# Optimization experiments

Measured on AMD Instinct MI355X. Metric: run time of the kernel, lower is better.

The kernel has to match this reference:

```python
import jax, jax.numpy as jnp
import numpy as np

C = 256          # conv_channels
C1 = C // 2      # 128
C2 = C // 4      # 64
G = 1            # relation_glimpse


def setup_inputs() -> dict:
    key = jax.random.key(0)
    ks = jax.random.split(key, 20)
    bs, Nr, in_dim, q_dim = 4, 256, 2052, 1024
    d_in = in_dim + 4  # pos (first 4 coords) re-appended
    s = 0.02
    inp = {
        "Q": jax.random.normal(ks[0], (bs, q_dim), jnp.float32),
        "X": jax.random.normal(ks[1], (bs, Nr, in_dim), jnp.float32),
        "Wv": jax.random.normal(ks[2], (d_in, C), jnp.float32) * s,
        "bv": jnp.zeros((C,), jnp.float32),
        "Wq": jax.random.normal(ks[3], (q_dim, C), jnp.float32) * s,
        "bq": jnp.zeros((C,), jnp.float32),
        # branch 0 (r_conv01/02/03): 1x1 convs == per-position dense
        "W01": jax.random.normal(ks[4], (C, C1), jnp.float32) * s,
        "b01": jnp.zeros((C1,), jnp.float32),
        "W02": jax.random.normal(ks[5], (C1, C2), jnp.float32) * s,
        "b02": jnp.zeros((C2,), jnp.float32),
        "W03": jax.random.normal(ks[6], (C2, G), jnp.float32) * s,
        "b03": jnp.zeros((G,), jnp.float32),
        # branch 1 (r_conv1/2/3): dilation on 1x1 kernels is a no-op
        "W1": jax.random.normal(ks[7], (C, C1), jnp.float32) * s,
        "b1": jnp.zeros((C1,), jnp.float32),
        "W2": jax.random.normal(ks[8], (C1, C2), jnp.float32) * s,
        "b2": jnp.zeros((C2,), jnp.float32),
        "W3": jax.random.normal(ks[9], (C2, G), jnp.float32) * s,
        "b3": jnp.zeros((G,), jnp.float32),
    }
    return inp


def _mlp3(P, Wa, ba, Wb, bb, Wc, bc):
    # P: [bs, Nr, Nr, C]; three 1x1-conv layers, ReLU after each (incl. last).
    h = jax.nn.relu(jnp.einsum("bijc,ck->bijk", P, Wa) + ba)
    h = jax.nn.relu(jnp.einsum("bijc,ck->bijk", h, Wb) + bb)
    h = jax.nn.relu(jnp.einsum("bijc,ck->bijk", h, Wc) + bc)
    return h[..., 0]  # [bs, Nr, Nr] (relation_glimpse == 1)


def _attn_map(h):
    # symmetrize, then softmax over all Nr*Nr positions
    s = h + jnp.swapaxes(h, 1, 2)
    bs, Nr, _ = s.shape
    return jax.nn.softmax(s.reshape(bs, Nr * Nr), axis=-1).reshape(bs, Nr, Nr)


def reference(Q, X, Wv, bv, Wq, bq, W01, b01, W02, b02, W03, b03,
              W1, b1, W2, b2, W3, b3):
    X_ = X
    # append pos (first 4 coords) -> [bs, Nr, in_dim+4]
    Xcat = jnp.concatenate([X, X[:, :, :4]], axis=2)
    Xp = jnp.einsum("bnd,dc->bnc", Xcat, Wv) + bv
    Qp = Q @ Wq + bq
    Xp = Xp + Qp[:, None, :]                       # [bs, Nr, C]
    P = Xp[:, None, :, :] * Xp[:, :, None, :]      # [bs, Nr, Nr, C] pairwise product
    m0 = _attn_map(_mlp3(P, W01, b01, W02, b02, W03, b03))
    m1 = _attn_map(_mlp3(P, W1, b1, W2, b2, W3, b3))
    # weighted aggregation with original features; /(2*glimpse), then sum over Nr
    rel = jnp.einsum("bij,bjd->bid", m0 + m1, X_) / (2.0 * G)
    return rel.sum(axis=1)  # [bs, in_dim]
```

## Files before the change

kernel.cpp:

```cpp
#include <hip/hip_runtime.h>
#include <hip/hip_bf16.h>

typedef __attribute__((ext_vector_type(8)))  short short8;
typedef __attribute__((ext_vector_type(4)))  float f32x4;
typedef __attribute__((ext_vector_type(16))) float f32x16;

#define NR 256
#define CC 256

__device__ __forceinline__ unsigned short f2bf(float x) {
    union { float f; unsigned int u; } v; v.f = x;
    unsigned int r = v.u + 0x7FFFu + ((v.u >> 16) & 1u);
    return (unsigned short)(r >> 16);
}

__device__ __forceinline__ unsigned int pk2bf(float a, float b) {
    __hip_bfloat162 h = __float22bfloat162_rn(make_float2(a, b));
    union { __hip_bfloat162 h; unsigned int u; } cv; cv.h = h;
    return cv.u;
}

__global__ __launch_bounds__(256) void qp_kernel(
    const float* __restrict__ Q, const float* __restrict__ Wq,
    float* __restrict__ Qpp)
{
    const int ksl = blockIdx.x, b = blockIdx.y;
    const int n = threadIdx.x;
    __shared__ float qs[256];
    qs[n] = Q[b * 1024 + ksl * 256 + n];
    __syncthreads();
    float acc = 0.f;
    #pragma unroll 4
    for (int d = 0; d < 256; ++d) acc += qs[d] * Wq[(size_t)(ksl * 256 + d) * 256 + n];
    Qpp[(ksl * 4 + b) * 256 + n] = acc;
}

__global__ __launch_bounds__(256) void wvp_pack_kernel(
    const float* __restrict__ Wv, unsigned short* __restrict__ wvp)
{
    __shared__ float tile[32][260];
    const int ks = blockIdx.x;
    const int tid = threadIdx.x;
    for (int idx = tid; idx < 32 * 256; idx += 256) {
        int cr = idx >> 8, n = idx & 255;
        int c = ks * 32 + cr;
        tile[cr][n] = (c < 2056) ? Wv[(size_t)c * 256 + n] : 0.f;
    }
    __syncthreads();
    #pragma unroll
    for (int q = 0; q < 4; ++q) {
        int t2 = tid * 4 + q;
        int nt = t2 >> 6, l = t2 & 63;
        int gg = l >> 4, jj = l & 15;
        short8 s;
        #pragma unroll
        for (int e = 0; e < 8; ++e)
            s[e] = (short)f2bf(tile[gg * 8 + e][nt * 16 + jj]);
        *(short8*)&wvp[((size_t)(ks * 16 + nt) * 64 + l) * 8] = s;
    }
}

__global__ __launch_bounds__(256) void pack_kernel(
    const float* __restrict__ W01, const float* __restrict__ W1,
    const float* __restrict__ W02, const float* __restrict__ W2,
    unsigned short* __restrict__ wpa, unsigned short* __restrict__ wpb)
{
    int t = blockIdx.x * 256 + threadIdx.x;
    if (t < 65536) {
        int e = t & 7, l = (t >> 3) & 63, ks = (t >> 9) & 15, nt = (t >> 13) & 3, br = (t >> 15) & 1;
        int cc = ks * 16 + (l >> 5) * 8 + e;
        int n = nt * 32 + (l & 31);
        const float* W = br ? W1 : W01;
        wpa[t] = f2bf(W[cc * 128 + n]);
    } else {
        int t2 = t - 65536;
        int e = t2 & 7, l = (t2 >> 3) & 63, ks = (t2 >> 9) & 7, nt = (t2 >> 12) & 1, br = (t2 >> 13) & 1;
        int cc = ks * 16 + (l >> 5) * 8 + e;
        int n = nt * 32 + (l & 31);
        const float* W = br ? W2 : W02;
        wpb[t2] = f2bf(W[cc * 64 + n]);
    }
}

__global__ __launch_bounds__(512) void xp_kernel(
    const float* __restrict__ X, const unsigned short* __restrict__ wvp,
    const float* __restrict__ bv, const float* __restrict__ bq,
    const float* __restrict__ Qpp, float* __restrict__ Xp)
{
    __shared__ f32x4 red[8][4][65];
    const int tid = threadIdx.x;
    const int w = tid >> 6;
    const int lane = tid & 63;
    const int g = lane >> 4, j16 = lane & 15;
    const int mt = blockIdx.x;
    const int bn = blockIdx.y;
    const int b  = blockIdx.z;

    const int i0 = mt * 16;
    const int n0 = bn * 64;
    const float* xrow = X + ((size_t)(b * NR) + (i0 + j16)) * 2052;

    f32x4 acc[4] = {};

    for (int ks = w; ks < 64; ks += 8) {
        const int c0 = ks * 32 + g * 8;
        float4 xa = *(const float4*)(xrow + c0);
        float4 xb = *(const float4*)(xrow + c0 + 4);
        union { short8 s; unsigned int u[4]; } af;
        af.u[0] = pk2bf(xa.x, xa.y);
        af.u[1] = pk2bf(xa.z, xa.w);
        af.u[2] = pk2bf(xb.x, xb.y);
        af.u[3] = pk2bf(xb.z, xb.w);
        #pragma unroll
        for (int nt = 0; nt < 4; ++nt) {
            short8 bf = ((const short8*)wvp)[(size_t)(ks * 16 + bn * 4 + nt) * 64 + lane];
            acc[nt] = __builtin_amdgcn_mfma_f32_16x16x32_bf16(af.s, bf, acc[nt], 0, 0, 0);
        }
    }
    if (w == 0) {
        float xv[8];
        #pragma unroll
        for (int e = 0; e < 8; ++e) {
            int q = g * 8 + e;
            int csrc = (q < 4) ? (2048 + q) : (q - 4);
            xv[e] = xrow[csrc];
        }
        union { short8 s; unsigned int u[4]; } af;
        af.u[0] = pk2bf(xv[0], xv[1]);
        af.u[1] = pk2bf(xv[2], xv[3]);
        af.u[2] = pk2bf(xv[4], xv[5]);
        af.u[3] = pk2bf(xv[6], xv[7]);
        #pragma unroll
        for (int nt = 0; nt < 4; ++nt) {
            short8 bf = ((const short8*)wvp)[(size_t)(64 * 16 + bn * 4 + nt) * 64 + lane];
            acc[nt] = __builtin_amdgcn_mfma_f32_16x16x32_bf16(af.s, bf, acc[nt], 0, 0, 0);
        }
    }
    #pragma unroll
    for (int nt = 0; nt < 4; ++nt) red[w][nt][lane] = acc[nt];
    __syncthreads();

    {
        int nt = tid >> 7;
        int l  = tid & 63;
        int half = (tid >> 6) & 1;
        float r0 = 0.f, r1 = 0.f;
        #pragma unroll
        for (int ww = 0; ww < 8; ++ww) {
            f32x4 v = red[ww][nt][l];
            r0 += v[half * 2 + 0];
            r1 += v[half * 2 + 1];
        }
        int gg = l >> 4, jj = l & 15;
        int n = n0 + nt * 16 + jj;
        float base = bv[n] + bq[n] + Qpp[b * 256 + n] + Qpp[(4 + b) * 256 + n]
                   + Qpp[(8 + b) * 256 + n] + Qpp[(12 + b) * 256 + n];
        int row0 = i0 + gg * 4 + half * 2;
        Xp[((b * NR) + row0) * CC + n]       = r0 + base;
        Xp[((b * NR) + row0 + 1) * CC + n]   = r1 + base;
    }
}

__global__ __launch_bounds__(256, 2) void pairs_kernel(
    const float* __restrict__ Xp,
    const unsigned short* __restrict__ wpa,
    const unsigned short* __restrict__ wpb,
    const float* __restrict__ b01, const float* __restrict__ b02,
    const float* __restrict__ b03,
    const float* __restrict__ b1,  const float* __restrict__ b2,
    const float* __restrict__ b3,
    const float* __restrict__ W03, const float* __restrict__ W3,
    float* __restrict__ colpart, float* __restrict__ rowpart)
{
    __shared__ __align__(16) unsigned short lds_wa[32768];
    __shared__ __align__(16) float lds_si[1024];
    __shared__ __align__(16) float lds_bias1[128];
    __shared__ __align__(16) float lds_bias2[64];
    __shared__ __align__(16) float lds_w3[64];
    __shared__ float lds_c[4][33];

    const int tid = threadIdx.x;
    const int wave = tid >> 6;
    const int lane = tid & 63;
    const int hi = lane >> 5;
    const int j32 = lane & 31;

    int bx = blockIdx.x;
    int b = bx / 288;
    int u = bx - b * 288;
    int k = 0, off = 0;
    while (u >= off + 8 * (8 - k)) { off += 8 * (8 - k); ++k; }
    int rel = u - off, wdt = 8 - k;
    int it = k * 8 + rel / wdt;
    int jt = k + rel % wdt;

    const int i0 = it * 4;
    const int i = i0 + wave;
    const int j0 = jt * 32;
    const int br4base = b;

    {
        int ww = tid >> 6, c4 = (tid & 63) * 4;
        *(float4*)&lds_si[ww * 256 + c4] =
            *(const float4*)&Xp[((b * NR) + (i0 + ww)) * CC + c4];
    }
    __syncthreads();

    const float* xr = Xp + ((size_t)(b * NR) + (j0 + j32)) * CC;
    const float* si = lds_si + wave * 256;
    short8 bfr[16];
    #pragma unroll
    for (int ks = 0; ks < 16; ++ks) {
        const int c0 = ks * 16 + hi * 8;
        float4 xa = *(const float4*)(xr + c0);
        float4 xb = *(const float4*)(xr + c0 + 4);
        float4 sa = *(const float4*)(si + c0);
        float4 sb = *(const float4*)(si + c0 + 4);
        union { short8 s; unsigned int u[4]; } f;
        f.u[0] = pk2bf(xa.x * sa.x, xa.y * sa.y);
        f.u[1] = pk2bf(xa.z * sa.z, xa.w * sa.w);
        f.u[2] = pk2bf(xb.x * sb.x, xb.y * sb.y);
        f.u[3] = pk2bf(xb.z * sb.z, xb.w * sb.w);
        bfr[ks] = f.s;
    }

    for (int br = 0; br < 2; ++br) {
        __syncthreads();
        {
            const uint4* gsrc = (const uint4*)(wpa + br * 32768);
            uint4* sdst = (uint4*)lds_wa;
            #pragma unroll
            for (int kk = 0; kk < 16; ++kk) sdst[kk * 256 + tid] = gsrc[kk * 256 + tid];
            if (tid < 128) lds_bias1[tid] = br ? b1[tid] : b01[tid];
            else if (tid < 192) lds_bias2[tid - 128] = br ? b2[tid - 128] : b02[tid - 128];
            else lds_w3[tid - 192] = br ? W3[tid - 192] : W03[tid - 192];
        }
        __syncthreads();
        const float b3v = br ? b3[0] : b03[0];

        f32x16 acc1[4];
        #pragma unroll
        for (int nt = 0; nt < 4; ++nt) {
            #pragma unroll
            for (int q = 0; q < 4; ++q) {
                f32x4 bb = *(const f32x4*)&lds_bias1[nt * 32 + q * 8 + hi * 4];
                acc1[nt][q * 4 + 0] = bb[0];
                acc1[nt][q * 4 + 1] = bb[1];
                acc1[nt][q * 4 + 2] = bb[2];
                acc1[nt][q * 4 + 3] = bb[3];
            }
        }
        #pragma unroll
        for (int ks = 0; ks < 16; ++ks) {
            #pragma unroll
            for (int nt = 0; nt < 4; ++nt) {
                short8 wf = ((const short8*)lds_wa)[(nt * 16 + ks) * 64 + lane];
                acc1[nt] = __builtin_amdgcn_mfma_f32_32x32x16_bf16(wf, bfr[ks], acc1[nt], 0, 0, 0);
            }
        }

        f32x16 acc2[2];
        #pragma unroll
        for (int nt = 0; nt < 2; ++nt) {
            #pragma unroll
            for (int q = 0; q < 4; ++q) {
                f32x4 bb = *(const f32x4*)&lds_bias2[nt * 32 + q * 8 + hi * 4];
                acc2[nt][q * 4 + 0] = bb[0];
                acc2[nt][q * 4 + 1] = bb[1];
                acc2[nt][q * 4 + 2] = bb[2];
                acc2[nt][q * 4 + 3] = bb[3];
            }
        }
        const short8* wb = (const short8*)wpb + (size_t)br * 16 * 64;
        #pragma unroll
        for (int t = 0; t < 4; ++t) {
            #pragma unroll
            for (int s = 0; s < 2; ++s) {
                const int bse = s * 8;
                float rA0 = fmaxf(acc1[t][bse + 0], 0.f), rA1 = fmaxf(acc1[t][bse + 1], 0.f);
                float rA2 = fmaxf(acc1[t][bse + 2], 0.f), rA3 = fmaxf(acc1[t][bse + 3], 0.f);
                float rB0 = fmaxf(acc1[t][bse + 4], 0.f), rB1 = fmaxf(acc1[t][bse + 5], 0.f);
                float rB2 = fmaxf(acc1[t][bse + 6], 0.f), rB3 = fmaxf(acc1[t][bse + 7], 0.f);
                unsigned int uA0 = pk2bf(rA0, rA1), uA1 = pk2bf(rA2, rA3);
                unsigned int uB0 = pk2bf(rB0, rB1), uB1 = pk2bf(rB2, rB3);
                unsigned int pA0 = __shfl_xor(uA0, 32, 64), pA1 = __shfl_xor(uA1, 32, 64);
                unsigned int pB0 = __shfl_xor(uB0, 32, 64), pB1 = __shfl_xor(uB1, 32, 64);
                union { short8 s8; unsigned int u[4]; } B2;
                B2.u[0] = hi ? pB0 : uA0;
                B2.u[1] = hi ? pB1 : uA1;
                B2.u[2] = hi ? uB0 : pA0;
                B2.u[3] = hi ? uB1 : pA1;
                const int ks2 = 2 * t + s;
                #pragma unroll
                for (int nt = 0; nt < 2; ++nt) {
                    short8 wf2 = wb[(nt * 8 + ks2) * 64 + lane];
                    acc2[nt] = __builtin_amdgcn_mfma_f32_32x32x16_bf16(wf2, B2.s8, acc2[nt], 0, 0, 0);
                }
            }
        }

        float part = 0.f;
        #pragma unroll
        for (int nt = 0; nt < 2; ++nt) {
            #pragma unroll
            for (int q = 0; q < 4; ++q) {
                f32x4 wv = *(const f32x4*)&lds_w3[nt * 32 + q * 8 + hi * 4];
                part += fmaxf(acc2[nt][q * 4 + 0], 0.f) * wv[0];
                part += fmaxf(acc2[nt][q * 4 + 1], 0.f) * wv[1];
                part += fmaxf(acc2[nt][q * 4 + 2], 0.f) * wv[2];
                part += fmaxf(acc2[nt][q * 4 + 3], 0.f) * wv[3];
            }
        }
        part += __shfl_xor(part, 32, 64);
        const float h3 = fmaxf(part + b3v, 0.f);
        const float E = __expf(2.f * h3);
        const int j = j0 + j32;
        const float Ec = (j >= i) ? E : 0.f;
        float Er = (j >  i) ? E : 0.f;

        Er += __shfl_xor(Er, 1, 64);
        Er += __shfl_xor(Er, 2, 64);
        Er += __shfl_xor(Er, 4, 64);
        Er += __shfl_xor(Er, 8, 64);
        Er += __shfl_xor(Er, 16, 64);
        Er += __shfl_xor(Er, 32, 64);
        if (lane == 0)
            rowpart[((size_t)(br * 4 + br4base) * NR + i) * 8 + jt] = 0.5f * Er;

        if (!hi) lds_c[wave][j32] = Ec;
        __syncthreads();
        if (tid < 32) {
            float c = lds_c[0][tid] + lds_c[1][tid] + lds_c[2][tid] + lds_c[3][tid];
            colpart[((size_t)(br * 4 + br4base) * NR + (j0 + tid)) * 64 + it] = c;
        }
    }
}

__global__ __launch_bounds__(256) void colsoft_final_kernel(
    const float* __restrict__ colpart, const float* __restrict__ rowpart,
    float* __restrict__ wn)
{
    const int blk = blockIdx.x;
    const int j = threadIdx.x;
    const int jt = j >> 5;
    float cs = 0.f;
    const float* cp = colpart + ((size_t)blk * NR + j) * 64;
    const int itmax = 8 * jt + 8;
    for (int it2 = 0; it2 < itmax; ++it2) cs += cp[it2];
    const float* rp = rowpart + ((size_t)blk * NR + j) * 8;
    for (int q = j >> 5; q < 8; ++q) cs += rp[q];

    __shared__ float red[256];
    red[j] = cs; __syncthreads();
    for (int s = 128; s > 0; s >>= 1) {
        if (j < s) red[j] += red[j + s];
        __syncthreads();
    }
    wn[blk * 256 + j] = cs / red[0];
}

__global__ __launch_bounds__(256) void agg_part_kernel(
    const float* __restrict__ X, const float* __restrict__ wn,
    float* __restrict__ apart)
{
    const int dc = blockIdx.x, b = blockIdx.y, jc = blockIdx.z;
    const int d = dc * 256 + threadIdx.x;
    __shared__ float wc[32];
    if (threadIdx.x < 32) {
        int j = jc * 32 + threadIdx.x;
        wc[threadIdx.x] = 0.5f * (wn[b * 256 + j] + wn[(4 + b) * 256 + j]);
    }
    __syncthreads();
    if (d < 2052) {
        const float* xp = X + (size_t)b * NR * 2052 + (size_t)jc * 32 * 2052 + d;
        float a0 = 0.f, a1 = 0.f, a2 = 0.f, a3 = 0.f;
        for (int r = 0; r < 32; r += 4) {
            a0 += wc[r + 0] * xp[(size_t)(r + 0) * 2052];
            a1 += wc[r + 1] * xp[(size_t)(r + 1) * 2052];
            a2 += wc[r + 2] * xp[(size_t)(r + 2) * 2052];
            a3 += wc[r + 3] * xp[(size_t)(r + 3) * 2052];
        }
        apart[(size_t)(jc * 4 + b) * 2304 + d] = (a0 + a1) + (a2 + a3);
    }
}

__global__ __launch_bounds__(256) void agg_final_kernel(
    const float* __restrict__ apart, float* __restrict__ out)
{
    const int dc = blockIdx.x, b = blockIdx.y;
    const int d = dc * 256 + threadIdx.x;
    if (d < 2052) {
        float s = 0.f;
        #pragma unroll
        for (int jc = 0; jc < 8; ++jc) s += apart[(size_t)(jc * 4 + b) * 2304 + d];
        out[b * 2052 + d] = s;
    }
}

extern "C" void kernel_launch(void* const* d_in, const int* in_sizes, int n_in,
                              void* d_out, int out_size, void* d_ws, size_t ws_size,
                              hipStream_t stream) {
    const float* Q   = (const float*)d_in[0];
    const float* X   = (const float*)d_in[1];
    const float* Wv  = (const float*)d_in[2];
    const float* bv  = (const float*)d_in[3];
    const float* Wq  = (const float*)d_in[4];
    const float* bq  = (const float*)d_in[5];
    const float* W01 = (const float*)d_in[6];
    const float* b01 = (const float*)d_in[7];
    const float* W02 = (const float*)d_in[8];
    const float* b02 = (const float*)d_in[9];
    const float* W03 = (const float*)d_in[10];
    const float* b03 = (const float*)d_in[11];
    const float* W1  = (const float*)d_in[12];
    const float* b1  = (const float*)d_in[13];
    const float* W2  = (const float*)d_in[14];
    const float* b2  = (const float*)d_in[15];
    const float* W3  = (const float*)d_in[16];
    const float* b3  = (const float*)d_in[17];

    char* ws = (char*)d_ws;
    float* Xp   = (float*)(ws + 0);
    float* Qpp  = (float*)(ws + 1048576);
    float* wn   = (float*)(ws + 1064960);
    unsigned short* wpa = (unsigned short*)(ws + 1073152);
    unsigned short* wpb = (unsigned short*)(ws + 1204224);
    float* colpart = (float*)(ws + 1236992);
    float* rowpart = (float*)(ws + 1761280);
    unsigned short* wvp = (unsigned short*)(ws + 1236992);
    float* apart = (float*)(ws + 0);
    float* out = (float*)d_out;

    qp_kernel<<<dim3(4, 4), 256, 0, stream>>>(Q, Wq, Qpp);
    wvp_pack_kernel<<<65, 256, 0, stream>>>(Wv, wvp);
    pack_kernel<<<320, 256, 0, stream>>>(W01, W1, W02, W2, wpa, wpb);
    xp_kernel<<<dim3(16, 4, 4), 512, 0, stream>>>(X, wvp, bv, bq, Qpp, Xp);
    pairs_kernel<<<1152, 256, 0, stream>>>(Xp, wpa, wpb, b01, b02, b03,
                                           b1, b2, b3, W03, W3, colpart, rowpart);
    colsoft_final_kernel<<<8, 256, 0, stream>>>(colpart, rowpart, wn);
    agg_part_kernel<<<dim3(9, 4, 8), 256, 0, stream>>>(X, wn, apart);
    agg_final_kernel<<<dim3(9, 4), 256, 0, stream>>>(apart, out);
}
```

Baseline: 111.9 us.

## Split pair MLP branches across blocks, merge setup kernels, narrow xp tiles

Merges the three setup kernels (Qp projection, Wv packing, MLP weight packing) into one launch. The xp projection now uses narrower 32-column tiles across twice as many blocks. The pairs kernel gives each branch its own block, doubling the grid. It stages only half of the first-layer weights in LDS (the rest is read from global memory) to allow four blocks per CU, and colpart is packed into a compact triangular layout. This trades redundant pairwise-product and Xp loads per branch and uncached global weight reads for more occupancy and parallelism, plus fewer launches.

```diff
diff --git a/kernel.cpp b/kernel.cpp
--- a/kernel.cpp
+++ b/kernel.cpp
@@ -20,65 +20,61 @@
     return cv.u;
 }
 
-__global__ __launch_bounds__(256) void qp_kernel(
-    const float* __restrict__ Q, const float* __restrict__ Wq,
-    float* __restrict__ Qpp)
-{
-    const int ksl = blockIdx.x, b = blockIdx.y;
-    const int n = threadIdx.x;
-    __shared__ float qs[256];
-    qs[n] = Q[b * 1024 + ksl * 256 + n];
-    __syncthreads();
-    float acc = 0.f;
-    #pragma unroll 4
-    for (int d = 0; d < 256; ++d) acc += qs[d] * Wq[(size_t)(ksl * 256 + d) * 256 + n];
-    Qpp[(ksl * 4 + b) * 256 + n] = acc;
-}
-
-__global__ __launch_bounds__(256) void wvp_pack_kernel(
-    const float* __restrict__ Wv, unsigned short* __restrict__ wvp)
-{
-    __shared__ float tile[32][260];
-    const int ks = blockIdx.x;
-    const int tid = threadIdx.x;
-    for (int idx = tid; idx < 32 * 256; idx += 256) {
-        int cr = idx >> 8, n = idx & 255;
-        int c = ks * 32 + cr;
-        tile[cr][n] = (c < 2056) ? Wv[(size_t)c * 256 + n] : 0.f;
-    }
-    __syncthreads();
-    #pragma unroll
-    for (int q = 0; q < 4; ++q) {
-        int t2 = tid * 4 + q;
-        int nt = t2 >> 6, l = t2 & 63;
-        int gg = l >> 4, jj = l & 15;
-        short8 s;
-        #pragma unroll
-        for (int e = 0; e < 8; ++e)
-            s[e] = (short)f2bf(tile[gg * 8 + e][nt * 16 + jj]);
-        *(short8*)&wvp[((size_t)(ks * 16 + nt) * 64 + l) * 8] = s;
-    }
-}
-
-__global__ __launch_bounds__(256) void pack_kernel(
+__global__ __launch_bounds__(256) void setup_kernel(
+    const float* __restrict__ Q, const float* __restrict__ Wq, float* __restrict__ Qpp,
+    const float* __restrict__ Wv, unsigned short* __restrict__ wvp,
     const float* __restrict__ W01, const float* __restrict__ W1,
     const float* __restrict__ W02, const float* __restrict__ W2,
     unsigned short* __restrict__ wpa, unsigned short* __restrict__ wpb)
 {
-    int t = blockIdx.x * 256 + threadIdx.x;
-    if (t < 65536) {
-        int e = t & 7, l = (t >> 3) & 63, ks = (t >> 9) & 15, nt = (t >> 13) & 3, br = (t >> 15) & 1;
-        int cc = ks * 16 + (l >> 5) * 8 + e;
-        int n = nt * 32 + (l & 31);
-        const float* W = br ? W1 : W01;
-        wpa[t] = f2bf(W[cc * 128 + n]);
+    __shared__ float tile[32][260];
+    __shared__ float qs[256];
+    const int bx = blockIdx.x;
+    const int tid = threadIdx.x;
+
+    if (bx < 16) {
+        int ksl = bx & 3, b = bx >> 2;
+        qs[tid] = Q[b * 1024 + ksl * 256 + tid];
+        __syncthreads();
+        float acc = 0.f;
+        #pragma unroll 4
+        for (int d = 0; d < 256; ++d) acc += qs[d] * Wq[(size_t)(ksl * 256 + d) * 256 + tid];
+        Qpp[(ksl * 4 + b) * 256 + tid] = acc;
+    } else if (bx < 81) {
+        int ks = bx - 16;
+        for (int idx = tid; idx < 32 * 256; idx += 256) {
+            int cr = idx >> 8, n = idx & 255;
+            int c = ks * 32 + cr;
+            tile[cr][n] = (c < 2056) ? Wv[(size_t)c * 256 + n] : 0.f;
+        }
+        __syncthreads();
+        #pragma unroll
+        for (int q = 0; q < 4; ++q) {
+            int t2 = tid * 4 + q;
+            int nt = t2 >> 6, l = t2 & 63;
+            int gg = l >> 4, jj = l & 15;
+            short8 s;
+            #pragma unroll
+            for (int e = 0; e < 8; ++e)
+                s[e] = (short)f2bf(tile[gg * 8 + e][nt * 16 + jj]);
+            *(short8*)&wvp[((size_t)(ks * 16 + nt) * 64 + l) * 8] = s;
+        }
     } else {
-        int t2 = t - 65536;
-        int e = t2 & 7, l = (t2 >> 3) & 63, ks = (t2 >> 9) & 7, nt = (t2 >> 12) & 1, br = (t2 >> 13) & 1;
-        int cc = ks * 16 + (l >> 5) * 8 + e;
-        int n = nt * 32 + (l & 31);
-        const float* W = br ? W2 : W02;
-        wpb[t2] = f2bf(W[cc * 64 + n]);
+        int t = (bx - 81) * 256 + tid;
+        if (t < 65536) {
+            int e = t & 7, l = (t >> 3) & 63, ks = (t >> 9) & 15, nt = (t >> 13) & 3, br = (t >> 15) & 1;
+            int cc = ks * 16 + (l >> 5) * 8 + e;
+            int n = nt * 32 + (l & 31);
+            const float* W = br ? W1 : W01;
+            wpa[t] = f2bf(W[cc * 128 + n]);
+        } else {
+            int t2 = t - 65536;
+            int e = t2 & 7, l = (t2 >> 3) & 63, ks = (t2 >> 9) & 7, nt = (t2 >> 12) & 1, br = (t2 >> 13) & 1;
+            int cc = ks * 16 + (l >> 5) * 8 + e;
+            int n = nt * 32 + (l & 31);
+            const float* W = br ? W2 : W02;
+            wpb[t2] = f2bf(W[cc * 64 + n]);
+        }
     }
 }
 
@@ -87,7 +83,7 @@
     const float* __restrict__ bv, const float* __restrict__ bq,
     const float* __restrict__ Qpp, float* __restrict__ Xp)
 {
-    __shared__ f32x4 red[8][4][65];
+    __shared__ f32x4 red[8][2][65];
     const int tid = threadIdx.x;
     const int w = tid >> 6;
     const int lane = tid & 63;
@@ -97,10 +93,10 @@
     const int b  = blockIdx.z;
 
     const int i0 = mt * 16;
-    const int n0 = bn * 64;
+    const int n0 = bn * 32;
     const float* xrow = X + ((size_t)(b * NR) + (i0 + j16)) * 2052;
 
-    f32x4 acc[4] = {};
+    f32x4 acc[2] = {};
 
     for (int ks = w; ks < 64; ks += 8) {
         const int c0 = ks * 32 + g * 8;
@@ -112,8 +108,8 @@
         af.u[2] = pk2bf(xb.x, xb.y);
         af.u[3] = pk2bf(xb.z, xb.w);
         #pragma unroll
-        for (int nt = 0; nt < 4; ++nt) {
-            short8 bf = ((const short8*)wvp)[(size_t)(ks * 16 + bn * 4 + nt) * 64 + lane];
+        for (int nt = 0; nt < 2; ++nt) {
+            short8 bf = ((const short8*)wvp)[(size_t)(ks * 16 + bn * 2 + nt) * 64 + lane];
             acc[nt] = __builtin_amdgcn_mfma_f32_16x16x32_bf16(af.s, bf, acc[nt], 0, 0, 0);
         }
     }
@@ -131,37 +127,33 @@
         af.u[2] = pk2bf(xv[4], xv[5]);
         af.u[3] = pk2bf(xv[6], xv[7]);
         #pragma unroll
-        for (int nt = 0; nt < 4; ++nt) {
-            short8 bf = ((const short8*)wvp)[(size_t)(64 * 16 + bn * 4 + nt) * 64 + lane];
+        for (int nt = 0; nt < 2; ++nt) {
+            short8 bf = ((const short8*)wvp)[(size_t)(64 * 16 + bn * 2 + nt) * 64 + lane];
             acc[nt] = __builtin_amdgcn_mfma_f32_16x16x32_bf16(af.s, bf, acc[nt], 0, 0, 0);
         }
     }
     #pragma unroll
-    for (int nt = 0; nt < 4; ++nt) red[w][nt][lane] = acc[nt];
+    for (int nt = 0; nt < 2; ++nt) red[w][nt][lane] = acc[nt];
     __syncthreads();
 
     {
-        int nt = tid >> 7;
-        int l  = tid & 63;
-        int half = (tid >> 6) & 1;
-        float r0 = 0.f, r1 = 0.f;
-        #pragma unroll
-        for (int ww = 0; ww < 8; ++ww) {
-            f32x4 v = red[ww][nt][l];
-            r0 += v[half * 2 + 0];
-            r1 += v[half * 2 + 1];
-        }
+        int nt  = tid >> 8;
+        int rem = tid & 255;
+        int l   = rem & 63;
+        int reg = (rem >> 6) & 3;
+        float r = 0.f;
+        #pragma unroll
+        for (int ww = 0; ww < 8; ++ww) r += red[ww][nt][l][reg];
         int gg = l >> 4, jj = l & 15;
         int n = n0 + nt * 16 + jj;
         float base = bv[n] + bq[n] + Qpp[b * 256 + n] + Qpp[(4 + b) * 256 + n]
                    + Qpp[(8 + b) * 256 + n] + Qpp[(12 + b) * 256 + n];
-        int row0 = i0 + gg * 4 + half * 2;
-        Xp[((b * NR) + row0) * CC + n]       = r0 + base;
-        Xp[((b * NR) + row0 + 1) * CC + n]   = r1 + base;
-    }
-}
-
-__global__ __launch_bounds__(256, 2) void pairs_kernel(
+        int row = i0 + gg * 4 + reg;
+        Xp[((b * NR) + row) * CC + n] = r + base;
+    }
+}
+
+__global__ __launch_bounds__(256, 4) void pairs_kernel(
     const float* __restrict__ Xp,
     const unsigned short* __restrict__ wpa,
     const unsigned short* __restrict__ wpb,
@@ -172,7 +164,7 @@
     const float* __restrict__ W03, const float* __restrict__ W3,
     float* __restrict__ colpart, float* __restrict__ rowpart)
 {
-    __shared__ __align__(16) unsigned short lds_wa[32768];
+    __shared__ __align__(16) unsigned short lds_wa[16384];
     __shared__ __align__(16) float lds_si[1024];
     __shared__ __align__(16) float lds_bias1[128];
     __shared__ __align__(16) float lds_bias2[64];
@@ -186,8 +178,10 @@
     const int j32 = lane & 31;
 
     int bx = blockIdx.x;
-    int b = bx / 288;
-    int u = bx - b * 288;
+    int b = bx / 576;
+    int r = bx - b * 576;
+    int br = r / 288;
+    int u = r - br * 288;
     int k = 0, off = 0;
     while (u >= off + 8 * (8 - k)) { off += 8 * (8 - k); ++k; }
     int rel = u - off, wdt = 8 - k;
@@ -197,14 +191,24 @@
     const int i0 = it * 4;
     const int i = i0 + wave;
     const int j0 = jt * 32;
-    const int br4base = b;
+    const int blk = br * 4 + b;
 
     {
-        int ww = tid >> 6, c4 = (tid & 63) * 4;
-        *(float4*)&lds_si[ww * 256 + c4] =
-            *(const float4*)&Xp[((b * NR) + (i0 + ww)) * CC + c4];
-    }
-    __syncthreads();
+        int c4 = lane * 4;
+        *(float4*)&lds_si[wave * 256 + c4] =
+            *(const float4*)&Xp[((b * NR) + i) * CC + c4];
+    }
+
+    {
+        const uint4* gsrc = (const uint4*)(wpa + (size_t)br * 32768);
+        uint4* sdst = (uint4*)lds_wa;
+        #pragma unroll
+        for (int kk = 0; kk < 8; ++kk) sdst[kk * 256 + tid] = gsrc[kk * 256 + tid];
+    }
+    if (tid < 128) lds_bias1[tid] = br ? b1[tid] : b01[tid];
+    else if (tid < 192) lds_bias2[tid - 128] = br ? b2[tid - 128] : b02[tid - 128];
+    else lds_w3[tid - 192] = br ? W3[tid - 192] : W03[tid - 192];
+    const float b3v = br ? b3[0] : b03[0];
 
     const float* xr = Xp + ((size_t)(b * NR) + (j0 + j32)) * CC;
     const float* si = lds_si + wave * 256;
@@ -224,115 +228,98 @@
         bfr[ks] = f.s;
     }
 
-    for (int br = 0; br < 2; ++br) {
-        __syncthreads();
-        {
-            const uint4* gsrc = (const uint4*)(wpa + br * 32768);
-            uint4* sdst = (uint4*)lds_wa;
-            #pragma unroll
-            for (int kk = 0; kk < 16; ++kk) sdst[kk * 256 + tid] = gsrc[kk * 256 + tid];
-            if (tid < 128) lds_bias1[tid] = br ? b1[tid] : b01[tid];
-            else if (tid < 192) lds_bias2[tid - 128] = br ? b2[tid - 128] : b02[tid - 128];
-            else lds_w3[tid - 192] = br ? W3[tid - 192] : W03[tid - 192];
-        }
-        __syncthreads();
-        const float b3v = br ? b3[0] : b03[0];
-
-        f32x16 acc1[4];
-        #pragma unroll
-        for (int nt = 0; nt < 4; ++nt) {
-            #pragma unroll
-            for (int q = 0; q < 4; ++q) {
-                f32x4 bb = *(const f32x4*)&lds_bias1[nt * 32 + q * 8 + hi * 4];
-                acc1[nt][q * 4 + 0] = bb[0];
-                acc1[nt][q * 4 + 1] = bb[1];
-                acc1[nt][q * 4 + 2] = bb[2];
-                acc1[nt][q * 4 + 3] = bb[3];
-            }
+    __syncthreads();
+
+    const short8* gwa = (const short8*)wpa + (size_t)br * 4096;
+    const short8* wb  = (const short8*)wpb + (size_t)br * 1024;
+
+    f32x16 acc2[2];
+    #pragma unroll
+    for (int nt = 0; nt < 2; ++nt) {
+        #pragma unroll
+        for (int q = 0; q < 4; ++q) {
+            const float* bb = &lds_bias2[nt * 32 + q * 8 + hi * 4];
+            acc2[nt][q * 4 + 0] = bb[0];
+            acc2[nt][q * 4 + 1] = bb[1];
+            acc2[nt][q * 4 + 2] = bb[2];
+            acc2[nt][q * 4 + 3] = bb[3];
+        }
+    }
+
+    #pragma unroll
+    for (int t = 0; t < 4; ++t) {
+        f32x16 acc1;
+        #pragma unroll
+        for (int q = 0; q < 4; ++q) {
+            const float* bb = &lds_bias1[t * 32 + q * 8 + hi * 4];
+            acc1[q * 4 + 0] = bb[0];
+            acc1[q * 4 + 1] = bb[1];
+            acc1[q * 4 + 2] = bb[2];
+            acc1[q * 4 + 3] = bb[3];
         }
         #pragma unroll
         for (int ks = 0; ks < 16; ++ks) {
-            #pragma unroll
-            for (int nt = 0; nt < 4; ++nt) {
-                short8 wf = ((const short8*)lds_wa)[(nt * 16 + ks) * 64 + lane];
-                acc1[nt] = __builtin_amdgcn_mfma_f32_32x32x16_bf16(wf, bfr[ks], acc1[nt], 0, 0, 0);
-            }
-        }
-
-        f32x16 acc2[2];
-        #pragma unroll
-        for (int nt = 0; nt < 2; ++nt) {
-            #pragma unroll
-            for (int q = 0; q < 4; ++q) {
-                f32x4 bb = *(const f32x4*)&lds_bias2[nt * 32 + q * 8 + hi * 4];
-                acc2[nt][q * 4 + 0] = bb[0];
-                acc2[nt][q * 4 + 1] = bb[1];
-                acc2[nt][q * 4 + 2] = bb[2];
-                acc2[nt][q * 4 + 3] = bb[3];
-            }
-        }
-        const short8* wb = (const short8*)wpb + (size_t)br * 16 * 64;
-        #pragma unroll
-        for (int t = 0; t < 4; ++t) {
-            #pragma unroll
-            for (int s = 0; s < 2; ++s) {
-                const int bse = s * 8;
-                float rA0 = fmaxf(acc1[t][bse + 0], 0.f), rA1 = fmaxf(acc1[t][bse + 1], 0.f);
-                float rA2 = fmaxf(acc1[t][bse + 2], 0.f), rA3 = fmaxf(acc1[t][bse + 3], 0.f);
-                float rB0 = fmaxf(acc1[t][bse + 4], 0.f), rB1 = fmaxf(acc1[t][bse + 5], 0.f);
-                float rB2 = fmaxf(acc1[t][bse + 6], 0.f), rB3 = fmaxf(acc1[t][bse + 7], 0.f);
-                unsigned int uA0 = pk2bf(rA0, rA1), uA1 = pk2bf(rA2, rA3);
-                unsigned int uB0 = pk2bf(rB0, rB1), uB1 = pk2bf(rB2, rB3);
-                unsigned int pA0 = __shfl_xor(uA0, 32, 64), pA1 = __shfl_xor(uA1, 32, 64);
-                unsigned int pB0 = __shfl_xor(uB0, 32, 64), pB1 = __shfl_xor(uB1, 32, 64);
-                union { short8 s8; unsigned int u[4]; } B2;
-                B2.u[0] = hi ? pB0 : uA0;
-                B2.u[1] = hi ? pB1 : uA1;
-                B2.u[2] = hi ? uB0 : pA0;
-                B2.u[3] = hi ? uB1 : pA1;
-                const int ks2 = 2 * t + s;
-                #pragma unroll
-                for (int nt = 0; nt < 2; ++nt) {
-                    short8 wf2 = wb[(nt * 8 + ks2) * 64 + lane];
-                    acc2[nt] = __builtin_amdgcn_mfma_f32_32x32x16_bf16(wf2, B2.s8, acc2[nt], 0, 0, 0);
-                }
-            }
-        }
-
-        float part = 0.f;
-        #pragma unroll
-        for (int nt = 0; nt < 2; ++nt) {
-            #pragma unroll
-            for (int q = 0; q < 4; ++q) {
-                f32x4 wv = *(const f32x4*)&lds_w3[nt * 32 + q * 8 + hi * 4];
-                part += fmaxf(acc2[nt][q * 4 + 0], 0.f) * wv[0];
-                part += fmaxf(acc2[nt][q * 4 + 1], 0.f) * wv[1];
-                part += fmaxf(acc2[nt][q * 4 + 2], 0.f) * wv[2];
-                part += fmaxf(acc2[nt][q * 4 + 3], 0.f) * wv[3];
-            }
-        }
-        part += __shfl_xor(part, 32, 64);
-        const float h3 = fmaxf(part + b3v, 0.f);
-        const float E = __expf(2.f * h3);
-        const int j = j0 + j32;
-        const float Ec = (j >= i) ? E : 0.f;
-        float Er = (j >  i) ? E : 0.f;
-
-        Er += __shfl_xor(Er, 1, 64);
-        Er += __shfl_xor(Er, 2, 64);
-        Er += __shfl_xor(Er, 4, 64);
-        Er += __shfl_xor(Er, 8, 64);
-        Er += __shfl_xor(Er, 16, 64);
-        Er += __shfl_xor(Er, 32, 64);
-        if (lane == 0)
-            rowpart[((size_t)(br * 4 + br4base) * NR + i) * 8 + jt] = 0.5f * Er;
-
-        if (!hi) lds_c[wave][j32] = Ec;
-        __syncthreads();
-        if (tid < 32) {
-            float c = lds_c[0][tid] + lds_c[1][tid] + lds_c[2][tid] + lds_c[3][tid];
-            colpart[((size_t)(br * 4 + br4base) * NR + (j0 + tid)) * 64 + it] = c;
-        }
+            short8 wf = (t < 2)
+                ? ((const short8*)lds_wa)[(t * 16 + ks) * 64 + lane]
+                : gwa[(t * 16 + ks) * 64 + lane];
+            acc1 = __builtin_amdgcn_mfma_f32_32x32x16_bf16(wf, bfr[ks], acc1, 0, 0, 0);
+        }
+        #pragma unroll
+        for (int s = 0; s < 2; ++s) {
+            const int bse = s * 8;
+            float rA0 = fmaxf(acc1[bse + 0], 0.f), rA1 = fmaxf(acc1[bse + 1], 0.f);
+            float rA2 = fmaxf(acc1[bse + 2], 0.f), rA3 = fmaxf(acc1[bse + 3], 0.f);
+            float rB0 = fmaxf(acc1[bse + 4], 0.f), rB1 = fmaxf(acc1[bse + 5], 0.f);
+            float rB2 = fmaxf(acc1[bse + 6], 0.f), rB3 = fmaxf(acc1[bse + 7], 0.f);
+            unsigned int uA0 = pk2bf(rA0, rA1), uA1 = pk2bf(rA2, rA3);
+            unsigned int uB0 = pk2bf(rB0, rB1), uB1 = pk2bf(rB2, rB3);
+            unsigned int pA0 = __shfl_xor(uA0, 32, 64), pA1 = __shfl_xor(uA1, 32, 64);
+            unsigned int pB0 = __shfl_xor(uB0, 32, 64), pB1 = __shfl_xor(uB1, 32, 64);
+            union { short8 s8; unsigned int u[4]; } B2;
+            B2.u[0] = hi ? pB0 : uA0;
+            B2.u[1] = hi ? pB1 : uA1;
+            B2.u[2] = hi ? uB0 : pA0;
+            B2.u[3] = hi ? uB1 : pA1;
+            const int ks2 = 2 * t + s;
+            acc2[0] = __builtin_amdgcn_mfma_f32_32x32x16_bf16(wb[ks2 * 64 + lane], B2.s8, acc2[0], 0, 0, 0);
+            acc2[1] = __builtin_amdgcn_mfma_f32_32x32x16_bf16(wb[(8 + ks2) * 64 + lane], B2.s8, acc2[1], 0, 0, 0);
+        }
+    }
+
+    float part = 0.f;
+    #pragma unroll
+    for (int nt = 0; nt < 2; ++nt) {
+        #pragma unroll
+        for (int q = 0; q < 4; ++q) {
+            const float* wv = &lds_w3[nt * 32 + q * 8 + hi * 4];
+            part += fmaxf(acc2[nt][q * 4 + 0], 0.f) * wv[0];
+            part += fmaxf(acc2[nt][q * 4 + 1], 0.f) * wv[1];
+            part += fmaxf(acc2[nt][q * 4 + 2], 0.f) * wv[2];
+            part += fmaxf(acc2[nt][q * 4 + 3], 0.f) * wv[3];
+        }
+    }
+    part += __shfl_xor(part, 32, 64);
+    const float h3 = fmaxf(part + b3v, 0.f);
+    const float E = __expf(2.f * h3);
+    const int j = j0 + j32;
+    const float Ec = (j >= i) ? E : 0.f;
+    float Er = (j >  i) ? E : 0.f;
+
+    Er += __shfl_xor(Er, 1, 64);
+    Er += __shfl_xor(Er, 2, 64);
+    Er += __shfl_xor(Er, 4, 64);
+    Er += __shfl_xor(Er, 8, 64);
+    Er += __shfl_xor(Er, 16, 64);
+    Er += __shfl_xor(Er, 32, 64);
+    if (lane == 0)
+        rowpart[((size_t)blk * NR + i) * 8 + jt] = 0.5f * Er;
+
+    if (!hi) lds_c[wave][j32] = Ec;
+    __syncthreads();
+    if (tid < 32) {
+        float c = lds_c[0][tid] + lds_c[1][tid] + lds_c[2][tid] + lds_c[3][tid];
+        const int cnt = 8 * jt + 8;
+        colpart[(size_t)blk * 9216 + 128 * jt * (jt + 1) + tid * cnt + it] = c;
     }
 }
 
@@ -342,13 +329,13 @@
 {
     const int blk = blockIdx.x;
     const int j = threadIdx.x;
-    const int jt = j >> 5;
+    const int jt = j >> 5, j32l = j & 31;
+    const int cnt = 8 * jt + 8;
     float cs = 0.f;
-    const float* cp = colpart + ((size_t)blk * NR + j) * 64;
-    const int itmax = 8 * jt + 8;
-    for (int it2 = 0; it2 < itmax; ++it2) cs += cp[it2];
+    const float* cp = colpart + (size_t)blk * 9216 + 128 * jt * (jt + 1) + j32l * cnt;
+    for (int it2 = 0; it2 < cnt; ++it2) cs += cp[it2];
     const float* rp = rowpart + ((size_t)blk * NR + j) * 8;
-    for (int q = j >> 5; q < 8; ++q) cs += rp[q];
+    for (int q = jt; q < 8; ++q) cs += rp[q];
 
     __shared__ float red[256];
     red[j] = cs; __syncthreads();
@@ -374,11 +361,11 @@
     if (d < 2052) {
         const float* xp = X + (size_t)b * NR * 2052 + (size_t)jc * 32 * 2052 + d;
         float a0 = 0.f, a1 = 0.f, a2 = 0.f, a3 = 0.f;
-        for (int r = 0; r < 32; r += 4) {
-            a0 += wc[r + 0] * xp[(size_t)(r + 0) * 2052];
-            a1 += wc[r + 1] * xp[(size_t)(r + 1) * 2052];
-            a2 += wc[r + 2] * xp[(size_t)(r + 2) * 2052];
-            a3 += wc[r + 3] * xp[(size_t)(r + 3) * 2052];
+        for (int rr = 0; rr < 32; rr += 4) {
+            a0 += wc[rr + 0] * xp[(size_t)(rr + 0) * 2052];
+            a1 += wc[rr + 1] * xp[(size_t)(rr + 1) * 2052];
+            a2 += wc[rr + 2] * xp[(size_t)(rr + 2) * 2052];
+            a3 += wc[rr + 3] * xp[(size_t)(rr + 3) * 2052];
         }
         apart[(size_t)(jc * 4 + b) * 2304 + d] = (a0 + a1) + (a2 + a3);
     }
@@ -426,16 +413,15 @@
     unsigned short* wpa = (unsigned short*)(ws + 1073152);
     unsigned short* wpb = (unsigned short*)(ws + 1204224);
     float* colpart = (float*)(ws + 1236992);
-    float* rowpart = (float*)(ws + 1761280);
+    float* rowpart = (float*)(ws + 1531904);
     unsigned short* wvp = (unsigned short*)(ws + 1236992);
     float* apart = (float*)(ws + 0);
     float* out = (float*)d_out;
 
-    qp_kernel<<<dim3(4, 4), 256, 0, stream>>>(Q, Wq, Qpp);
-    wvp_pack_kernel<<<65, 256, 0, stream>>>(Wv, wvp);
-    pack_kernel<<<320, 256, 0, stream>>>(W01, W1, W02, W2, wpa, wpb);
-    xp_kernel<<<dim3(16, 4, 4), 512, 0, stream>>>(X, wvp, bv, bq, Qpp, Xp);
-    pairs_kernel<<<1152, 256, 0, stream>>>(Xp, wpa, wpb, b01, b02, b03,
+    setup_kernel<<<401, 256, 0, stream>>>(Q, Wq, Qpp, Wv, wvp,
+                                          W01, W1, W02, W2, wpa, wpb);
+    xp_kernel<<<dim3(16, 8, 4), 512, 0, stream>>>(X, wvp, bv, bq, Qpp, Xp);
+    pairs_kernel<<<2304, 256, 0, stream>>>(Xp, wpa, wpb, b01, b02, b03,
                                            b1, b2, b3, W03, W3, colpart, rowpart);
     colsoft_final_kernel<<<8, 256, 0, stream>>>(colpart, rowpart, wn);
     agg_part_kernel<<<dim3(9, 4, 8), 256, 0, stream>>>(X, wn, apart);
```

New measurement: 131.7 us. +17.7%, slower.
